# Performance work log

Measured on AMD Instinct MI355X. Metric: run time of the kernel, lower is better.

## Reference

```python
import jax, jax.numpy as jnp
import numpy as np


def _init_boxes(C, F, max_h, max_w, seed=0):
    # Mirrors BoxConv2d.reset_parameters: random centers/sizes in pixel units,
    # then normalized by max_input_h / max_input_w (reparametrize).
    rng = np.random.default_rng(seed)
    min_h = min_w = 2.0
    ch = rng.uniform(-max_h * 2 / 4.8 + 1 + min_h / 2, max_h * 2 / 4.8 - 1 - min_h / 2, (C, F))
    cw = rng.uniform(-max_w * 2 / 4.8 + 1 + min_w / 2, max_w * 2 / 4.8 - 1 - min_w / 2, (C, F))
    hh = 2.0 * rng.uniform(min_h / 2, np.minimum(max_h - 1 - ch, ch + max_h - 1))
    ww = 2.0 * rng.uniform(min_w / 2, np.minimum(max_w - 1 - cw, cw + max_w - 1))
    x_min = (ch - hh / 2) / max_h
    x_max = (ch + hh / 2) / max_h
    y_min = (cw - ww / 2) / max_w
    y_max = (cw + ww / 2) / max_w
    return [jnp.asarray(a, jnp.float32) for a in (x_min, x_max, y_min, y_max)]


def setup_inputs() -> dict:
    key = jax.random.key(0)
    B, C, F, H, W = 8, 32, 8, 128, 128
    x = jax.random.normal(key, (B, C, H, W), dtype=jnp.float32)
    x_min, x_max, y_min, y_max = _init_boxes(C, F, H, W)
    return {"input": x, "x_min": x_min, "x_max": x_max, "y_min": y_min,
            "y_max": y_max, "max_input_h": H, "max_input_w": W}


def reference(input, x_min, x_max, y_min, y_max, max_input_h, max_input_w):
    # Exact box convolution: out[b, c*F+f, h, w] = continuous-area sum of
    # input[b, c] over rectangle [h+xm, h+xM+1] x [w+ym, w+yM+1], computed
    # by bilinear interpolation of the integral image (fractional corners).
    B, C, H, W = input.shape
    F = x_min.shape[1]
    dt = input.dtype
    # stored params are normalized; recover pixel-unit coordinates
    xm = x_min * max_input_h
    xM = x_max * max_input_h
    ym = y_min * max_input_w
    yM = y_max * max_input_w
    # integral image: I[b,c,i,j] = sum of input over rows<i, cols<j  -> [B,C,H+1,W+1]
    I = jnp.pad(jnp.cumsum(jnp.cumsum(input, axis=2), axis=3),
                ((0, 0), (0, 0), (1, 0), (1, 0)))
    h = jnp.arange(H, dtype=dt)
    w = jnp.arange(W, dtype=dt)
    Hf = jnp.asarray(H, dt)
    Wf = jnp.asarray(W, dt)
    u0 = jnp.clip(h[None, None, :] + xm[:, :, None], 0.0, Hf)        # [C,F,H]
    u1 = jnp.clip(h[None, None, :] + xM[:, :, None] + 1.0, 0.0, Hf)  # [C,F,H]
    v0 = jnp.clip(w[None, None, :] + ym[:, :, None], 0.0, Wf)        # [C,F,W]
    v1 = jnp.clip(w[None, None, :] + yM[:, :, None] + 1.0, 0.0, Wf)  # [C,F,W]

    Ie = I[:, :, None, :, :]  # [B,C,1,H+1,W+1]

    def row_interp(u):  # u: [C,F,H] -> [B,C,F,H,W+1]
        i0 = jnp.clip(jnp.floor(u), 0.0, Hf - 1.0)
        a = (u - i0)[None, :, :, :, None]
        i0 = i0.astype(jnp.int32)[None, :, :, :, None]
        g0 = jnp.take_along_axis(Ie, i0, axis=3)
        g1 = jnp.take_along_axis(Ie, i0 + 1, axis=3)
        return (1.0 - a) * g0 + a * g1

    # row-differenced, row-interpolated integral image
    Drow = row_interp(u1) - row_interp(u0)  # [B,C,F,H,W+1]

    def col_interp(v):  # v: [C,F,W] -> [B,C,F,H,W]
        j0 = jnp.clip(jnp.floor(v), 0.0, Wf - 1.0)
        b = (v - j0)[None, :, :, None, :]
        j0 = j0.astype(jnp.int32)[None, :, :, None, :]
        g0 = jnp.take_along_axis(Drow, j0, axis=4)
        g1 = jnp.take_along_axis(Drow, j0 + 1, axis=4)
        return (1.0 - b) * g0 + b * g1

    out = col_interp(v1) - col_interp(v0)  # [B,C,F,H,W]
    return out.reshape(B, C * F, H, W)
```

## Files before the change

kernel.cpp:

```cpp
#include <hip/hip_runtime.h>


__global__ __launch_bounds__(1024, 4)
void boxconv_kernel(const float* __restrict__ in,
                    const float* __restrict__ x_min,
                    const float* __restrict__ x_max,
                    const float* __restrict__ y_min,
                    const float* __restrict__ y_max,
                    float* __restrict__ out)
{
    constexpr int H = 128, W = 128, C = 32, F = 8;
    constexpr int STRIDE = 132;
    constexpr int NROW = 129;

    __shared__ float I[NROW * STRIDE];
    __shared__ float Dbuf[16][2 * STRIDE];

    const int tid  = threadIdx.x;
    const int lane = tid & 63;
    const int wid  = tid >> 6;
    const int bc   = blockIdx.x;
    const int c    = bc & 31;

    if (tid < NROW)                    I[tid * STRIDE] = 0.f;
    else if (tid >= 256 && tid < 256 + STRIDE - 1) I[tid - 255] = 0.f;
    __syncthreads();

    const float* img = in + (size_t)bc * (H * W);
    if (tid < H) {
        const int r = tid;
        const float4* row4 = (const float4*)(img + r * W);
        float* Irow = I + (r + 1) * STRIDE + 1;
        float acc = 0.f;
        #pragma unroll 8
        for (int w4 = 0; w4 < W / 4; ++w4) {
            float4 v = row4[w4];
            float s0 = acc + v.x;
            float s1 = s0 + v.y;
            float s2 = s1 + v.z;
            float s3 = s2 + v.w;
            Irow[w4 * 4 + 0] = s0;
            Irow[w4 * 4 + 1] = s1;
            Irow[w4 * 4 + 2] = s2;
            Irow[w4 * 4 + 3] = s3;
            acc = s3;
        }
    }
    __syncthreads();

    if (tid < W) {
        const int cc = tid + 1;
        float acc = 0.f;
        for (int chunk = 0; chunk < 4; ++chunk) {
            const int r0 = 1 + chunk * 32;
            float v[32];
            #pragma unroll
            for (int i = 0; i < 32; ++i) v[i] = I[(r0 + i) * STRIDE + cc];
            #pragma unroll
            for (int i = 0; i < 32; ++i) { acc += v[i]; v[i] = acc; }
            #pragma unroll
            for (int i = 0; i < 32; ++i) I[(r0 + i) * STRIDE + cc] = v[i];
        }
    }
    __syncthreads();

    const int f     = wid >> 1;
    const int hbase = (wid & 1) * 64;

    const float xm = x_min[c * F + f] * 128.f;
    const float xM = x_max[c * F + f] * 128.f;
    const float ym = y_min[c * F + f] * 128.f;
    const float yM = y_max[c * F + f] * 128.f;

    int   j0[2], j1[2];
    float b0v[2], b1v[2], cb0[2], cb1[2];
    #pragma unroll
    for (int k = 0; k < 2; ++k) {
        const float wf = (float)(lane + 64 * k);
        const float v0 = fminf(fmaxf(wf + ym, 0.f), 128.f);
        const float v1 = fminf(fmaxf(wf + yM + 1.f, 0.f), 128.f);
        const float j0f = fminf(floorf(v0), 127.f);
        const float j1f = fminf(floorf(v1), 127.f);
        j0[k] = (int)j0f;  j1[k] = (int)j1f;
        b0v[k] = v0 - j0f; b1v[k] = v1 - j1f;
        cb0[k] = 1.f - b0v[k]; cb1[k] = 1.f - b1v[k];
    }

    const int rsub = lane >> 5;
    const int wp   = (lane & 31) * 4;
    float* Dw = Dbuf[wid];
    float* outf = out + ((size_t)bc * F + f) * (H * W);

    for (int it = 0; it < 32; ++it) {
        const int h = hbase + it * 2;

        const float hf = (float)(h + rsub);
        const float u0 = fminf(fmaxf(hf + xm, 0.f), 128.f);
        const float u1 = fminf(fmaxf(hf + xM + 1.f, 0.f), 128.f);
        const float i0f = fminf(floorf(u0), 127.f);
        const float i1f = fminf(floorf(u1), 127.f);
        const int   i0  = (int)i0f, i1 = (int)i1f;
        const float a0 = u0 - i0f, a1 = u1 - i1f;
        const float ca0 = 1.f - a0, ca1 = 1.f - a1;

        const float* p0 = I + i0 * STRIDE;
        const float* p1 = I + i1 * STRIDE;
        const float4 q0  = *(const float4*)(p0 + wp);
        const float4 q0b = *(const float4*)(p0 + STRIDE + wp);
        const float4 q1  = *(const float4*)(p1 + wp);
        const float4 q1b = *(const float4*)(p1 + STRIDE + wp);
        float4 d;
        d.x = ca1 * q1.x + a1 * q1b.x - ca0 * q0.x - a0 * q0b.x;
        d.y = ca1 * q1.y + a1 * q1b.y - ca0 * q0.y - a0 * q0b.y;
        d.z = ca1 * q1.z + a1 * q1b.z - ca0 * q0.z - a0 * q0b.z;
        d.w = ca1 * q1.w + a1 * q1b.w - ca0 * q0.w - a0 * q0b.w;
        *(float4*)(Dw + rsub * STRIDE + wp) = d;
        if ((lane & 31) == 31) {
            Dw[rsub * STRIDE + 128] =
                ca1 * p1[128] + a1 * p1[STRIDE + 128]
              - ca0 * p0[128] - a0 * p0[STRIDE + 128];
        }

        #pragma unroll
        for (int rr = 0; rr < 2; ++rr) {
            const float* Dr = Dw + rr * STRIDE;
            #pragma unroll
            for (int k = 0; k < 2; ++k) {
                const float Dj0  = Dr[j0[k]];
                const float Dj0p = Dr[j0[k] + 1];
                const float Dj1  = Dr[j1[k]];
                const float Dj1p = Dr[j1[k] + 1];
                outf[(h + rr) * W + lane + 64 * k] =
                    cb1[k] * Dj1 + b1v[k] * Dj1p - cb0[k] * Dj0 - b0v[k] * Dj0p;
            }
        }
    }
}

extern "C" void kernel_launch(void* const* d_in, const int* in_sizes, int n_in,
                              void* d_out, int out_size, void* d_ws, size_t ws_size,
                              hipStream_t stream) {
    const float* in    = (const float*)d_in[0];
    const float* x_min = (const float*)d_in[1];
    const float* x_max = (const float*)d_in[2];
    const float* y_min = (const float*)d_in[3];
    const float* y_max = (const float*)d_in[4];
    float* outp = (float*)d_out;

    boxconv_kernel<<<dim3(8 * 32), dim3(1024), 0, stream>>>(
        in, x_min, x_max, y_min, y_max, outp);
}
```

Before: 157.5 us.

## Split filters across two blocks, precompute tail column, software-pipeline row loads

Each (b,c) image now runs on two 512-thread blocks that each handle half of the filters, doubling the grid from 256 to 512 blocks. That fills more CUs, at the cost of computing the integral image twice. The last-column row-interpolation values are precomputed once per wave into a small LDS tail buffer. The main loop prefetches the next row pair's integral-image loads before writing the current outputs, to hide LDS latency.

```diff
diff --git a/kernel.cpp b/kernel.cpp
--- a/kernel.cpp
+++ b/kernel.cpp
@@ -1,7 +1,11 @@
 #include <hip/hip_runtime.h>
 
 
-__global__ __launch_bounds__(1024, 4)
+constexpr int H = 128, W = 128, C = 32, F = 8;
+constexpr int STRIDE = 132;
+constexpr int NROW = 129;
+
+__global__ __launch_bounds__(512, 4)
 void boxconv_kernel(const float* __restrict__ in,
                     const float* __restrict__ x_min,
                     const float* __restrict__ x_max,
@@ -9,36 +13,31 @@
                     const float* __restrict__ y_max,
                     float* __restrict__ out)
 {
-    constexpr int H = 128, W = 128, C = 32, F = 8;
-    constexpr int STRIDE = 132;
-    constexpr int NROW = 129;
-
     __shared__ float I[NROW * STRIDE];
-    __shared__ float Dbuf[16][2 * STRIDE];
+    __shared__ float Dbuf[8][2 * STRIDE];
+    __shared__ float Dtail[8][64];
 
     const int tid  = threadIdx.x;
     const int lane = tid & 63;
     const int wid  = tid >> 6;
-    const int bc   = blockIdx.x;
-    const int c    = bc & 31;
 
-    if (tid < NROW)                    I[tid * STRIDE] = 0.f;
-    else if (tid >= 256 && tid < 256 + STRIDE - 1) I[tid - 255] = 0.f;
+    const int bc     = blockIdx.x >> 1;
+    const int half_f = blockIdx.x & 1;
+    const int c      = bc & 31;
+
+    if (tid < NROW) I[tid * STRIDE] = 0.f;
+    else if (tid < NROW + STRIDE - 1) I[tid - 128] = 0.f;
     __syncthreads();
 
     const float* img = in + (size_t)bc * (H * W);
     if (tid < H) {
-        const int r = tid;
-        const float4* row4 = (const float4*)(img + r * W);
-        float* Irow = I + (r + 1) * STRIDE + 1;
+        const float4* row4 = (const float4*)(img + tid * W);
+        float* Irow = I + (tid + 1) * STRIDE + 1;
         float acc = 0.f;
         #pragma unroll 8
         for (int w4 = 0; w4 < W / 4; ++w4) {
             float4 v = row4[w4];
-            float s0 = acc + v.x;
-            float s1 = s0 + v.y;
-            float s2 = s1 + v.z;
-            float s3 = s2 + v.w;
+            float s0 = acc + v.x, s1 = s0 + v.y, s2 = s1 + v.z, s3 = s2 + v.w;
             Irow[w4 * 4 + 0] = s0;
             Irow[w4 * 4 + 1] = s1;
             Irow[w4 * 4 + 2] = s2;
@@ -64,7 +63,8 @@
     }
     __syncthreads();
 
-    const int f     = wid >> 1;
+    const int fi    = wid >> 1;
+    const int f     = half_f * 4 + fi;
     const int hbase = (wid & 1) * 64;
 
     const float xm = x_min[c * F + f] * 128.f;
@@ -73,7 +73,7 @@
     const float yM = y_max[c * F + f] * 128.f;
 
     int   j0[2], j1[2];
-    float b0v[2], b1v[2], cb0[2], cb1[2];
+    float b1v[2], cb1[2], nb0v[2], ncb0[2];
     #pragma unroll
     for (int k = 0; k < 2; ++k) {
         const float wf = (float)(lane + 64 * k);
@@ -82,56 +82,89 @@
         const float j0f = fminf(floorf(v0), 127.f);
         const float j1f = fminf(floorf(v1), 127.f);
         j0[k] = (int)j0f;  j1[k] = (int)j1f;
-        b0v[k] = v0 - j0f; b1v[k] = v1 - j1f;
-        cb0[k] = 1.f - b0v[k]; cb1[k] = 1.f - b1v[k];
+        const float b0 = v0 - j0f, b1 = v1 - j1f;
+        b1v[k] = b1; cb1[k] = 1.f - b1;
+        nb0v[k] = -b0; ncb0[k] = -(1.f - b0);
     }
 
     const int rsub = lane >> 5;
     const int wp   = (lane & 31) * 4;
     float* Dw = Dbuf[wid];
-    float* outf = out + ((size_t)bc * F + f) * (H * W);
+    float* Dt = Dtail[wid];
 
-    for (int it = 0; it < 32; ++it) {
-        const int h = hbase + it * 2;
-
+    auto rowCoef = [&](int h, const float*& p0, const float*& p1,
+                       float& a0, float& a1, float& ca0, float& ca1) {
         const float hf = (float)(h + rsub);
         const float u0 = fminf(fmaxf(hf + xm, 0.f), 128.f);
         const float u1 = fminf(fmaxf(hf + xM + 1.f, 0.f), 128.f);
         const float i0f = fminf(floorf(u0), 127.f);
         const float i1f = fminf(floorf(u1), 127.f);
-        const int   i0  = (int)i0f, i1 = (int)i1f;
+        a0 = u0 - i0f; a1 = u1 - i1f; ca0 = 1.f - a0; ca1 = 1.f - a1;
+        p0 = I + (int)i0f * STRIDE;
+        p1 = I + (int)i1f * STRIDE;
+    };
+
+    {
+        const float hf = (float)(hbase + lane);
+        const float u0 = fminf(fmaxf(hf + xm, 0.f), 128.f);
+        const float u1 = fminf(fmaxf(hf + xM + 1.f, 0.f), 128.f);
+        const float i0f = fminf(floorf(u0), 127.f);
+        const float i1f = fminf(floorf(u1), 127.f);
+        const int i0 = (int)i0f, i1 = (int)i1f;
         const float a0 = u0 - i0f, a1 = u1 - i1f;
-        const float ca0 = 1.f - a0, ca1 = 1.f - a1;
+        const float t = (1.f - a1) * I[i1 * STRIDE + 128] + a1 * I[(i1 + 1) * STRIDE + 128]
+                      - (1.f - a0) * I[i0 * STRIDE + 128] - a0 * I[(i0 + 1) * STRIDE + 128];
+        Dt[(lane & 1) * 32 + (lane >> 1)] = t;
+    }
 
-        const float* p0 = I + i0 * STRIDE;
-        const float* p1 = I + i1 * STRIDE;
-        const float4 q0  = *(const float4*)(p0 + wp);
-        const float4 q0b = *(const float4*)(p0 + STRIDE + wp);
-        const float4 q1  = *(const float4*)(p1 + wp);
-        const float4 q1b = *(const float4*)(p1 + STRIDE + wp);
+    float* outf = out + ((size_t)bc * F + f) * (size_t)(H * W);
+
+    const float *p0, *p1;
+    float a0, a1, ca0, ca1;
+    rowCoef(hbase, p0, p1, a0, a1, ca0, ca1);
+    float4 q0  = *(const float4*)(p0 + wp);
+    float4 q0b = *(const float4*)(p0 + STRIDE + wp);
+    float4 q1  = *(const float4*)(p1 + wp);
+    float4 q1b = *(const float4*)(p1 + STRIDE + wp);
+
+    for (int it = 0; it < 32; ++it) {
+        const int h = hbase + it * 2;
+
         float4 d;
         d.x = ca1 * q1.x + a1 * q1b.x - ca0 * q0.x - a0 * q0b.x;
         d.y = ca1 * q1.y + a1 * q1b.y - ca0 * q0.y - a0 * q0b.y;
         d.z = ca1 * q1.z + a1 * q1b.z - ca0 * q0.z - a0 * q0b.z;
         d.w = ca1 * q1.w + a1 * q1b.w - ca0 * q0.w - a0 * q0b.w;
         *(float4*)(Dw + rsub * STRIDE + wp) = d;
-        if ((lane & 31) == 31) {
-            Dw[rsub * STRIDE + 128] =
-                ca1 * p1[128] + a1 * p1[STRIDE + 128]
-              - ca0 * p0[128] - a0 * p0[STRIDE + 128];
-        }
+        if ((lane & 31) == 31) Dw[rsub * STRIDE + 128] = Dt[rsub * 32 + it];
 
+        float Dj0[2][2], Dj0p[2][2], Dj1[2][2], Dj1p[2][2];
         #pragma unroll
         for (int rr = 0; rr < 2; ++rr) {
             const float* Dr = Dw + rr * STRIDE;
             #pragma unroll
             for (int k = 0; k < 2; ++k) {
-                const float Dj0  = Dr[j0[k]];
-                const float Dj0p = Dr[j0[k] + 1];
-                const float Dj1  = Dr[j1[k]];
-                const float Dj1p = Dr[j1[k] + 1];
-                outf[(h + rr) * W + lane + 64 * k] =
-                    cb1[k] * Dj1 + b1v[k] * Dj1p - cb0[k] * Dj0 - b0v[k] * Dj0p;
+                const float* pj0 = Dr + j0[k];
+                const float* pj1 = Dr + j1[k];
+                Dj0[rr][k] = pj0[0]; Dj0p[rr][k] = pj0[1];
+                Dj1[rr][k] = pj1[0]; Dj1p[rr][k] = pj1[1];
+            }
+        }
+
+        rowCoef(h + 2, p0, p1, a0, a1, ca0, ca1);
+        q0  = *(const float4*)(p0 + wp);
+        q0b = *(const float4*)(p0 + STRIDE + wp);
+        q1  = *(const float4*)(p1 + wp);
+        q1b = *(const float4*)(p1 + STRIDE + wp);
+
+        #pragma unroll
+        for (int rr = 0; rr < 2; ++rr) {
+            float* orow = outf + (size_t)(h + rr) * W;
+            #pragma unroll
+            for (int k = 0; k < 2; ++k) {
+                const float o = cb1[k] * Dj1[rr][k] + b1v[k] * Dj1p[rr][k]
+                              + ncb0[k] * Dj0[rr][k] + nb0v[k] * Dj0p[rr][k];
+                orow[lane + 64 * k] = o;
             }
         }
     }
@@ -147,6 +180,6 @@
     const float* y_max = (const float*)d_in[4];
     float* outp = (float*)d_out;
 
-    boxconv_kernel<<<dim3(8 * 32), dim3(1024), 0, stream>>>(
+    boxconv_kernel<<<dim3(8 * 32 * 2), dim3(512), 0, stream>>>(
         in, x_min, x_max, y_min, y_max, outp);
 }
```

Result: no change. 155.3 us (-1.4%).
